# Optimization experiments

Measured on AMD Instinct MI355X. Metric: run time of the kernel, lower is better.

## Reference

```python
import jax, jax.numpy as jnp
import numpy as np

B, T, C = 2, 2048, 1024
N_HEAD = 16
HEAD_DIM = C // N_HEAD


def setup_inputs() -> dict:
    key = jax.random.key(0)
    k1, k2, k3, k4, k5 = jax.random.split(key, 5)
    s = 1.0 / np.sqrt(C)
    return {
        "x": jax.random.normal(k1, (B, T, C), dtype=jnp.float32),
        "w_attn": jax.random.normal(k2, (C, 3 * C), dtype=jnp.float32) * s,
        "b_attn": jax.random.normal(k3, (3 * C,), dtype=jnp.float32) * 0.02,
        "w_proj": jax.random.normal(k4, (C, C), dtype=jnp.float32) * s,
        "b_proj": jax.random.normal(k5, (C,), dtype=jnp.float32) * 0.02,
    }


def reference(x, w_attn, b_attn, w_proj, b_proj):
    Bx, Tx, Cx = x.shape
    qkv = x @ w_attn + b_attn  # [B, T, 3C]
    q, k, v = jnp.split(qkv, 3, axis=2)
    # [B, H, T, D]
    q = q.reshape(Bx, Tx, N_HEAD, HEAD_DIM).transpose(0, 2, 1, 3)
    k = k.reshape(Bx, Tx, N_HEAD, HEAD_DIM).transpose(0, 2, 1, 3)
    v = v.reshape(Bx, Tx, N_HEAD, HEAD_DIM).transpose(0, 2, 1, 3)
    scale = 1.0 / jnp.sqrt(jnp.asarray(HEAD_DIM, dtype=x.dtype))
    att = jnp.einsum("bhqd,bhkd->bhqk", q, k) * scale  # [B,H,T,T]
    causal = jnp.tril(jnp.ones((Tx, Tx), dtype=bool))
    att = jnp.where(causal[None, None, :, :], att, -jnp.inf)
    att = jax.nn.softmax(att, axis=-1)
    y = jnp.einsum("bhqk,bhkd->bhqd", att, v)  # [B,H,T,D]
    y = y.transpose(0, 2, 1, 3).reshape(Bx, Tx, Cx)
    return y @ w_proj + b_proj
```

## Files before the change

kernel.cpp:

```cpp
#include <hip/hip_runtime.h>
#include <hip/hip_bf16.h>
#include <stdint.h>

#define TT 2048
#define CC 1024
#define NH 16
#define HD 64
#define BT 4096

typedef float f32x4 __attribute__((ext_vector_type(4)));
typedef __bf16 bf16x8 __attribute__((ext_vector_type(8)));
typedef __bf16 bf16x4 __attribute__((ext_vector_type(4)));
typedef short sh4 __attribute__((ext_vector_type(4)));

#define MFMA(a, b, c) __builtin_amdgcn_mfma_f32_16x16x32_bf16((a), (b), (c), 0, 0, 0)
#define MFMA16(a, b, c) __builtin_amdgcn_mfma_f32_16x16x16bf16_1k((a), (b), (c), 0, 0, 0)

__device__ __forceinline__ void gload16(const void* g, void* l) {
    __builtin_amdgcn_global_load_lds(
        (const __attribute__((address_space(1))) void*)g,
        (__attribute__((address_space(3))) void*)l,
        16, 0, 0);
}

__global__ __launch_bounds__(256) void prep(
    const float* __restrict__ x, __bf16* __restrict__ xb,
    const float* __restrict__ wa, __bf16* __restrict__ oa,
    const float* __restrict__ wp, __bf16* __restrict__ op) {
    __shared__ float tile[32][33];
    int b0 = blockIdx.x;
    if (b0 < 1024) {
        int i = b0 * 256 + threadIdx.x;
        const int stride = 1024 * 256;
        const int n4 = BT * CC / 4;
        for (; i < n4; i += stride) {
            float4 v = reinterpret_cast<const float4*>(x)[i];
            bf16x4 o;
            o.x = (__bf16)v.x; o.y = (__bf16)v.y;
            o.z = (__bf16)v.z; o.w = (__bf16)v.w;
            reinterpret_cast<bf16x4*>(xb)[i] = o;
        }
    } else {
        int idx = b0 - 1024;
        int bx = idx & 127, r0 = (idx >> 7) * 32;
        const float* in;
        __bf16* out;
        int C;
        if (bx < 96) { in = wa; out = oa; C = 3072; }
        else         { in = wp; out = op; C = 1024; bx -= 96; }
        int c0 = bx * 32;
        int tx = threadIdx.x & 31, ty = (threadIdx.x >> 5) & 7;
#pragma unroll
        for (int j = 0; j < 32; j += 8)
            tile[ty + j][tx] = in[(size_t)(r0 + ty + j) * C + c0 + tx];
        __syncthreads();
#pragma unroll
        for (int j = 0; j < 32; j += 8)
            out[(size_t)(c0 + ty + j) * 1024 + r0 + tx] = (__bf16)tile[tx][ty + j];
    }
}

template <int MODE>
__global__ __launch_bounds__(256) void gemm128(
    const __bf16* __restrict__ A, const __bf16* __restrict__ Bt,
    const float* __restrict__ bias,
    __bf16* __restrict__ oq, __bf16* __restrict__ ok, __bf16* __restrict__ ov,
    float* __restrict__ of, int M, int N, int K) {
    __shared__ __align__(16) __bf16 As[128 * 64];
    __shared__ __align__(16) __bf16 Bs[128 * 64];
    const int tid = threadIdx.x;
    const int w = tid >> 6, lane = tid & 63;
    const int l15 = lane & 15, lg = lane >> 4;
    const int m0 = blockIdx.y * 128, n0 = blockIdx.x * 128;
    const int wr = w >> 1, wc = w & 1;

    const f32x4 zero4 = {0.f, 0.f, 0.f, 0.f};
    f32x4 acc[4][4];
#pragma unroll
    for (int m = 0; m < 4; ++m)
#pragma unroll
        for (int n = 0; n < 4; ++n) acc[m][n] = zero4;

    const char* Ab = (const char*)A;
    const char* Bb = (const char*)Bt;
    const size_t rowbytes = (size_t)K * 2;

    for (int kt = 0; kt < K; kt += 64) {
#pragma unroll
        for (int j = 0; j < 4; ++j) {
            int base = (w * 4 + j) * 1024;
            int d0 = base + lane * 16;
            int row = d0 >> 7;
            int colb = d0 & 127;
            int scolb = colb ^ ((row & 7) << 4);
            gload16(Ab + (size_t)(m0 + row) * rowbytes + (size_t)kt * 2 + scolb,
                    (char*)As + base);
            gload16(Bb + (size_t)(n0 + row) * rowbytes + (size_t)kt * 2 + scolb,
                    (char*)Bs + base);
        }
        __syncthreads();
#pragma unroll
        for (int kk = 0; kk < 2; ++kk) {
            bf16x8 af[4], bfr[4];
#pragma unroll
            for (int m = 0; m < 4; ++m) {
                int row = wr * 64 + m * 16 + l15;
                int colb = kk * 64 + lg * 16;
                af[m] = *(const bf16x8*)((const char*)As + row * 128 +
                                         (colb ^ ((row & 7) << 4)));
            }
#pragma unroll
            for (int n = 0; n < 4; ++n) {
                int row = wc * 64 + n * 16 + l15;
                int colb = kk * 64 + lg * 16;
                bfr[n] = *(const bf16x8*)((const char*)Bs + row * 128 +
                                          (colb ^ ((row & 7) << 4)));
            }
#pragma unroll
            for (int m = 0; m < 4; ++m)
#pragma unroll
                for (int n = 0; n < 4; ++n)
                    acc[m][n] = MFMA(af[m], bfr[n], acc[m][n]);
        }
        __syncthreads();
    }

#pragma unroll
    for (int n = 0; n < 4; ++n) {
        int col = n0 + wc * 64 + n * 16 + l15;
        float bs = bias[col];
        if constexpr (MODE == 0) {
            int sec = col >> 10;
            int cc = col & 1023;
            int h = cc >> 6, d = cc & 63;
            if (sec == 2) {
#pragma unroll
                for (int m = 0; m < 4; ++m) {
                    int rowb = m0 + wr * 64 + m * 16 + lg * 4;
                    int bb = rowb >> 11, t = rowb & 2047;
                    bf16x4 pk;
#pragma unroll
                    for (int r = 0; r < 4; ++r) pk[r] = (__bf16)(acc[m][n][r] + bs);
                    size_t base = ((size_t)(bb * NH + h) * HD + d) * (TT * 2);
                    size_t byte = base + (size_t)((t & ~63) * 2 +
                                   (((t & 63) * 2) ^ ((d & 15) << 3)));
                    *(bf16x4*)((char*)ov + byte) = pk;
                }
            } else {
                __bf16* dst = (sec == 0) ? oq : ok;
                float mult = (sec == 0) ? 0.125f * 1.44269504088896340736f : 1.0f;
#pragma unroll
                for (int m = 0; m < 4; ++m) {
                    int rowb = m0 + wr * 64 + m * 16 + lg * 4;
#pragma unroll
                    for (int r = 0; r < 4; ++r) {
                        int row = rowb + r;
                        int bb = row >> 11, t = row & 2047;
                        float val = (acc[m][n][r] + bs) * mult;
                        dst[((size_t)(bb * NH + h) * TT + t) * HD + d] = (__bf16)val;
                    }
                }
            }
        } else {
#pragma unroll
            for (int m = 0; m < 4; ++m) {
                int rowb = m0 + wr * 64 + m * 16 + lg * 4;
#pragma unroll
                for (int r = 0; r < 4; ++r) {
                    int row = rowb + r;
                    of[(size_t)row * N + col] = acc[m][n][r] + bs;
                }
            }
        }
    }
}

__global__ __launch_bounds__(256) void attn_kernel(
    const __bf16* __restrict__ q, const __bf16* __restrict__ k,
    const __bf16* __restrict__ vt, __bf16* __restrict__ y) {
    __shared__ __align__(16) __bf16 Kb[2][64 * 64];
    __shared__ __align__(16) __bf16 Vb[2][64 * 64];

    const int n = blockIdx.x;
    const int batch = n >> 8, a = (n >> 5) & 7;
    const int qt = (batch == 0) ? 31 - a : (batch == 1) ? 16 + a
                 : (batch == 2) ? 15 - a : a;
    const int bh = ((n & 7) << 2) | ((n >> 3) & 3);
    const int tid = threadIdx.x, w = tid >> 6, lane = tid & 63;
    const int l15 = lane & 15, lg = lane >> 4;
    const char* kh = (const char*)(k + (size_t)bh * TT * HD);
    const char* vh = (const char*)(vt + (size_t)bh * HD * TT);
    const __bf16* qh = q + (size_t)bh * TT * HD;
    const int qbw = qt * 64 + w * 16;

    const f32x4 zero4 = {0.f, 0.f, 0.f, 0.f};
    float lrun = 0.f;
    f32x4 oacc[4];
    bf16x8 qf[2];
#pragma unroll
    for (int f = 0; f < 4; ++f) oacc[f] = zero4;
#pragma unroll
    for (int kk = 0; kk < 2; ++kk)
        qf[kk] = *(const bf16x8*)&qh[(size_t)(qbw + l15) * HD + kk * 32 + lg * 8];

    auto stage = [&](int kvb, int buf) {
#pragma unroll
        for (int j = 0; j < 2; ++j) {
            int d0 = ((w * 2 + j) * 64 + lane) * 16;
            int row = d0 >> 7, colb = d0 & 127;
            gload16(kh + (size_t)(kvb + row) * 128 + (colb ^ ((row & 7) << 4)),
                    (char*)Kb[buf] + d0);
            gload16(vh + (size_t)row * (TT * 2) + (size_t)kvb * 2 + colb,
                    (char*)Vb[buf] + d0);
        }
    };

    stage(0, 0);
    __syncthreads();

    for (int g = 0; g <= qt; ++g) {
        const int cur = g & 1;
        if (g < qt) stage((g + 1) * 64, cur ^ 1);
        const int kb = g * 64;

        f32x4 s[4];
#pragma unroll
        for (int kf = 0; kf < 4; ++kf) s[kf] = zero4;
        __builtin_amdgcn_s_setprio(1);
#pragma unroll
        for (int kf = 0; kf < 4; ++kf) {
            int krow = kf * 16 + l15;
            const char* kr = (const char*)Kb[cur] + krow * 128;
            bf16x8 k0 = *(const bf16x8*)(kr + ((lg * 16) ^ ((krow & 7) << 4)));
            bf16x8 k1 = *(const bf16x8*)(kr + ((64 + lg * 16) ^ ((krow & 7) << 4)));
            s[kf] = MFMA(k0, qf[0], s[kf]);
            s[kf] = MFMA(k1, qf[1], s[kf]);
        }
        __builtin_amdgcn_s_setprio(0);
        if (g == qt) {
            const int qq = qbw + l15;
#pragma unroll
            for (int kf = 0; kf < 4; ++kf)
#pragma unroll
                for (int r = 0; r < 4; ++r) {
                    int kk_ = kb + kf * 16 + lg * 4 + r;
                    if (kk_ > qq) s[kf][r] = -1e30f;
                }
        }
        float ss = 0.f;
        sh4 pb[4];
#pragma unroll
        for (int kf = 0; kf < 4; ++kf) {
            bf16x4 pk;
#pragma unroll
            for (int r = 0; r < 4; ++r) {
                float p = exp2f(s[kf][r]);
                pk[r] = (__bf16)p;
                ss += p;
            }
            pb[kf] = __builtin_bit_cast(sh4, pk);
        }
        lrun += ss;
        __builtin_amdgcn_s_setprio(1);
#pragma unroll
        for (int kf = 0; kf < 4; ++kf) {
            int cb = (kf * 32 + lg * 8) ^ (l15 << 3);
#pragma unroll
            for (int f = 0; f < 4; ++f) {
                int vrow = f * 16 + l15;
                bf16x4 va = *(const bf16x4*)((const char*)Vb[cur] + vrow * 128 + cb);
                oacc[f] = MFMA16(__builtin_bit_cast(sh4, va), pb[kf], oacc[f]);
            }
        }
        __builtin_amdgcn_s_setprio(0);
        __syncthreads();
    }

    lrun += __shfl_xor(lrun, 16);
    lrun += __shfl_xor(lrun, 32);
    const int b = bh >> 4, h = bh & 15;
    float inv = 1.0f / lrun;
#pragma unroll
    for (int f = 0; f < 4; ++f) {
        bf16x4 pk;
#pragma unroll
        for (int r = 0; r < 4; ++r) pk[r] = (__bf16)(oacc[f][r] * inv);
        *(bf16x4*)&y[(size_t)(b * TT + qbw + l15) * CC + h * 64 + f * 16 +
                     lg * 4] = pk;
    }
}

extern "C" void kernel_launch(void* const* d_in, const int* in_sizes, int n_in,
                              void* d_out, int out_size, void* d_ws, size_t ws_size,
                              hipStream_t stream) {
    const float* x      = (const float*)d_in[0];
    const float* w_attn = (const float*)d_in[1];
    const float* b_attn = (const float*)d_in[2];
    const float* w_proj = (const float*)d_in[3];
    const float* b_proj = (const float*)d_in[4];
    float* out = (float*)d_out;

    char* ws = (char*)d_ws;
    size_t off = 0;
    auto alloc = [&](size_t bytes) {
        char* p = ws + off;
        off += (bytes + 255) & ~(size_t)255;
        return p;
    };
    __bf16* xb   = (__bf16*)alloc((size_t)BT * CC * 2);
    __bf16* watb = (__bf16*)alloc((size_t)3 * CC * CC * 2);
    __bf16* wptb = (__bf16*)alloc((size_t)CC * CC * 2);
    __bf16* qb   = (__bf16*)alloc((size_t)BT * CC * 2);
    __bf16* kbuf = (__bf16*)alloc((size_t)BT * CC * 2);
    __bf16* vtb  = (__bf16*)alloc((size_t)BT * CC * 2);
    __bf16* yb   = (__bf16*)alloc((size_t)BT * CC * 2);

    prep<<<5120, 256, 0, stream>>>(x, xb, w_attn, watb, w_proj, wptb);

    gemm128<0><<<dim3(3 * CC / 128, BT / 128), 256, 0, stream>>>(
        xb, watb, b_attn, qb, kbuf, vtb, nullptr, BT, 3 * CC, CC);

    attn_kernel<<<1024, 256, 0, stream>>>(qb, kbuf, vtb, yb);

    gemm128<1><<<dim3(CC / 128, BT / 128), 256, 0, stream>>>(
        yb, wptb, b_proj, nullptr, nullptr, nullptr, out, BT, CC, CC);
}
```

Before: 108.7 us.

## Process two query tiles per attention block to reuse staged K/V tiles

Each attention workgroup now handles a 128-row query tile split into two 64-row sub-tiles. Every K/V tile staged in shared memory is reused for both sub-tiles, which roughly halves K/V global loads and LDS reads per query row, and the grid drops from 1024 to 512 blocks. The cost is doubled accumulator and score register use, which may lower occupancy, and the diagonal tile now runs extra masked compute for the lower sub-tile. The block-to-tile ordering is changed to keep causal workloads balanced.

```diff
diff --git a/kernel.cpp b/kernel.cpp
--- a/kernel.cpp
+++ b/kernel.cpp
@@ -182,31 +182,35 @@
     __shared__ __align__(16) __bf16 Vb[2][64 * 64];
 
     const int n = blockIdx.x;
-    const int batch = n >> 8, a = (n >> 5) & 7;
-    const int qt = (batch == 0) ? 31 - a : (batch == 1) ? 16 + a
-                 : (batch == 2) ? 15 - a : a;
+    const int j = n >> 5;
+    const int qt2 = (j < 8) ? 15 - j : j - 8;
     const int bh = ((n & 7) << 2) | ((n >> 3) & 3);
     const int tid = threadIdx.x, w = tid >> 6, lane = tid & 63;
     const int l15 = lane & 15, lg = lane >> 4;
     const char* kh = (const char*)(k + (size_t)bh * TT * HD);
     const char* vh = (const char*)(vt + (size_t)bh * HD * TT);
     const __bf16* qh = q + (size_t)bh * TT * HD;
-    const int qbw = qt * 64 + w * 16;
+    const int qbw[2] = { qt2 * 128 + w * 16, qt2 * 128 + 64 + w * 16 };
+    const int nt = 2 * qt2 + 2;
 
     const f32x4 zero4 = {0.f, 0.f, 0.f, 0.f};
-    float lrun = 0.f;
-    f32x4 oacc[4];
-    bf16x8 qf[2];
-#pragma unroll
-    for (int f = 0; f < 4; ++f) oacc[f] = zero4;
-#pragma unroll
-    for (int kk = 0; kk < 2; ++kk)
-        qf[kk] = *(const bf16x8*)&qh[(size_t)(qbw + l15) * HD + kk * 32 + lg * 8];
+    float lrun[2] = {0.f, 0.f};
+    f32x4 oacc[2][4];
+    bf16x8 qf[2][2];
+#pragma unroll
+    for (int a = 0; a < 2; ++a) {
+#pragma unroll
+        for (int f = 0; f < 4; ++f) oacc[a][f] = zero4;
+#pragma unroll
+        for (int kk = 0; kk < 2; ++kk)
+            qf[a][kk] = *(const bf16x8*)&qh[(size_t)(qbw[a] + l15) * HD +
+                                           kk * 32 + lg * 8];
+    }
 
     auto stage = [&](int kvb, int buf) {
 #pragma unroll
-        for (int j = 0; j < 2; ++j) {
-            int d0 = ((w * 2 + j) * 64 + lane) * 16;
+        for (int jj = 0; jj < 2; ++jj) {
+            int d0 = ((w * 2 + jj) * 64 + lane) * 16;
             int row = d0 >> 7, colb = d0 & 127;
             gload16(kh + (size_t)(kvb + row) * 128 + (colb ^ ((row & 7) << 4)),
                     (char*)Kb[buf] + d0);
@@ -218,14 +222,16 @@
     stage(0, 0);
     __syncthreads();
 
-    for (int g = 0; g <= qt; ++g) {
+    for (int g = 0; g < nt; ++g) {
         const int cur = g & 1;
-        if (g < qt) stage((g + 1) * 64, cur ^ 1);
+        if (g + 1 < nt) stage((g + 1) * 64, cur ^ 1);
         const int kb = g * 64;
 
-        f32x4 s[4];
-#pragma unroll
-        for (int kf = 0; kf < 4; ++kf) s[kf] = zero4;
+        f32x4 s[2][4];
+#pragma unroll
+        for (int a = 0; a < 2; ++a)
+#pragma unroll
+            for (int kf = 0; kf < 4; ++kf) s[a][kf] = zero4;
         __builtin_amdgcn_s_setprio(1);
 #pragma unroll
         for (int kf = 0; kf < 4; ++kf) {
@@ -233,34 +239,42 @@
             const char* kr = (const char*)Kb[cur] + krow * 128;
             bf16x8 k0 = *(const bf16x8*)(kr + ((lg * 16) ^ ((krow & 7) << 4)));
             bf16x8 k1 = *(const bf16x8*)(kr + ((64 + lg * 16) ^ ((krow & 7) << 4)));
-            s[kf] = MFMA(k0, qf[0], s[kf]);
-            s[kf] = MFMA(k1, qf[1], s[kf]);
+            s[0][kf] = MFMA(k0, qf[0][0], s[0][kf]);
+            s[0][kf] = MFMA(k1, qf[0][1], s[0][kf]);
+            s[1][kf] = MFMA(k0, qf[1][0], s[1][kf]);
+            s[1][kf] = MFMA(k1, qf[1][1], s[1][kf]);
         }
         __builtin_amdgcn_s_setprio(0);
-        if (g == qt) {
-            const int qq = qbw + l15;
-#pragma unroll
-            for (int kf = 0; kf < 4; ++kf)
+#pragma unroll
+        for (int a = 0; a < 2; ++a) {
+            if (kb + 63 > qbw[a]) {
+                const int qq = qbw[a] + l15;
+#pragma unroll
+                for (int kf = 0; kf < 4; ++kf)
+#pragma unroll
+                    for (int r = 0; r < 4; ++r) {
+                        int kk_ = kb + kf * 16 + lg * 4 + r;
+                        if (kk_ > qq) s[a][kf][r] = -1e30f;
+                    }
+            }
+        }
+        sh4 pb[2][4];
+#pragma unroll
+        for (int a = 0; a < 2; ++a) {
+            float ss0 = 0.f, ss1 = 0.f;
+#pragma unroll
+            for (int kf = 0; kf < 4; ++kf) {
+                bf16x4 pk;
 #pragma unroll
                 for (int r = 0; r < 4; ++r) {
-                    int kk_ = kb + kf * 16 + lg * 4 + r;
-                    if (kk_ > qq) s[kf][r] = -1e30f;
+                    float p = exp2f(s[a][kf][r]);
+                    pk[r] = (__bf16)p;
+                    if (kf & 1) ss1 += p; else ss0 += p;
                 }
-        }
-        float ss = 0.f;
-        sh4 pb[4];
-#pragma unroll
-        for (int kf = 0; kf < 4; ++kf) {
-            bf16x4 pk;
-#pragma unroll
-            for (int r = 0; r < 4; ++r) {
-                float p = exp2f(s[kf][r]);
-                pk[r] = (__bf16)p;
-                ss += p;
-            }
-            pb[kf] = __builtin_bit_cast(sh4, pk);
-        }
-        lrun += ss;
+                pb[a][kf] = __builtin_bit_cast(sh4, pk);
+            }
+            lrun[a] += ss0 + ss1;
+        }
         __builtin_amdgcn_s_setprio(1);
 #pragma unroll
         for (int kf = 0; kf < 4; ++kf) {
@@ -269,24 +283,30 @@
             for (int f = 0; f < 4; ++f) {
                 int vrow = f * 16 + l15;
                 bf16x4 va = *(const bf16x4*)((const char*)Vb[cur] + vrow * 128 + cb);
-                oacc[f] = MFMA16(__builtin_bit_cast(sh4, va), pb[kf], oacc[f]);
+                sh4 vs = __builtin_bit_cast(sh4, va);
+                oacc[0][f] = MFMA16(vs, pb[0][kf], oacc[0][f]);
+                oacc[1][f] = MFMA16(vs, pb[1][kf], oacc[1][f]);
             }
         }
         __builtin_amdgcn_s_setprio(0);
         __syncthreads();
     }
 
-    lrun += __shfl_xor(lrun, 16);
-    lrun += __shfl_xor(lrun, 32);
     const int b = bh >> 4, h = bh & 15;
-    float inv = 1.0f / lrun;
-#pragma unroll
-    for (int f = 0; f < 4; ++f) {
-        bf16x4 pk;
-#pragma unroll
-        for (int r = 0; r < 4; ++r) pk[r] = (__bf16)(oacc[f][r] * inv);
-        *(bf16x4*)&y[(size_t)(b * TT + qbw + l15) * CC + h * 64 + f * 16 +
-                     lg * 4] = pk;
+#pragma unroll
+    for (int a = 0; a < 2; ++a) {
+        float lr = lrun[a];
+        lr += __shfl_xor(lr, 16);
+        lr += __shfl_xor(lr, 32);
+        float inv = 1.0f / lr;
+#pragma unroll
+        for (int f = 0; f < 4; ++f) {
+            bf16x4 pk;
+#pragma unroll
+            for (int r = 0; r < 4; ++r) pk[r] = (__bf16)(oacc[a][f][r] * inv);
+            *(bf16x4*)&y[(size_t)(b * TT + qbw[a] + l15) * CC + h * 64 + f * 16 +
+                         lg * 4] = pk;
+        }
     }
 }
 
@@ -320,7 +340,7 @@
     gemm128<0><<<dim3(3 * CC / 128, BT / 128), 256, 0, stream>>>(
         xb, watb, b_attn, qb, kbuf, vtb, nullptr, BT, 3 * CC, CC);
 
-    attn_kernel<<<1024, 256, 0, stream>>>(qb, kbuf, vtb, yb);
+    attn_kernel<<<512, 256, 0, stream>>>(qb, kbuf, vtb, yb);
 
     gemm128<1><<<dim3(CC / 128, BT / 128), 256, 0, stream>>>(
         yb, wptb, b_proj, nullptr, nullptr, nullptr, out, BT, CC, CC);
```

Result: slower. 128.8 us (+18.5%).

## Split heavy causal query tiles across two blocks and combine partial outputs

Applied to the files above, without the earlier changes.

Query tiles 16-31 have the longest causal KV ranges, and each is now split into two blocks that each cover half of the KV range. Each half writes unnormalized partial outputs and row sums to scratch space that reuses the xb/watb buffers. A new combine kernel sums the two halves and normalizes them. The aim is to balance load across the 1536 blocks and shorten the tail. In exchange it adds an extra launch, scratch traffic, and bf16 rounding of the partial sums. The split relies on the running softmax using no running max, so partial sums can simply be added.

```diff
diff --git a/kernel.cpp b/kernel.cpp
--- a/kernel.cpp
+++ b/kernel.cpp
@@ -177,15 +177,28 @@
 
 __global__ __launch_bounds__(256) void attn_kernel(
     const __bf16* __restrict__ q, const __bf16* __restrict__ k,
-    const __bf16* __restrict__ vt, __bf16* __restrict__ y) {
+    const __bf16* __restrict__ vt, __bf16* __restrict__ y,
+    __bf16* __restrict__ opart, float* __restrict__ lpart) {
     __shared__ __align__(16) __bf16 Kb[2][64 * 64];
     __shared__ __align__(16) __bf16 Vb[2][64 * 64];
 
     const int n = blockIdx.x;
-    const int batch = n >> 8, a = (n >> 5) & 7;
-    const int qt = (batch == 0) ? 31 - a : (batch == 1) ? 16 + a
-                 : (batch == 2) ? 15 - a : a;
     const int bh = ((n & 7) << 2) | ((n >> 3) & 3);
+    const int u = n >> 5;
+    int qt, g0, g1, half;
+    const bool heavy = (u < 32);
+    if (heavy) {
+        qt = 16 + (u >> 1);
+        half = u & 1;
+        int n0 = (qt + 2) >> 1;
+        g0 = half ? n0 : 0;
+        g1 = half ? qt + 1 : n0;
+    } else {
+        qt = 47 - u;
+        half = 0;
+        g0 = 0;
+        g1 = qt + 1;
+    }
     const int tid = threadIdx.x, w = tid >> 6, lane = tid & 63;
     const int l15 = lane & 15, lg = lane >> 4;
     const char* kh = (const char*)(k + (size_t)bh * TT * HD);
@@ -215,12 +228,12 @@
         }
     };
 
-    stage(0, 0);
+    stage(g0 * 64, 0);
     __syncthreads();
 
-    for (int g = 0; g <= qt; ++g) {
-        const int cur = g & 1;
-        if (g < qt) stage((g + 1) * 64, cur ^ 1);
+    for (int g = g0; g < g1; ++g) {
+        const int cur = (g - g0) & 1;
+        if (g + 1 < g1) stage((g + 1) * 64, cur ^ 1);
         const int kb = g * 64;
 
         f32x4 s[4];
@@ -278,16 +291,62 @@
 
     lrun += __shfl_xor(lrun, 16);
     lrun += __shfl_xor(lrun, 32);
-    const int b = bh >> 4, h = bh & 15;
-    float inv = 1.0f / lrun;
-#pragma unroll
-    for (int f = 0; f < 4; ++f) {
-        bf16x4 pk;
-#pragma unroll
-        for (int r = 0; r < 4; ++r) pk[r] = (__bf16)(oacc[f][r] * inv);
-        *(bf16x4*)&y[(size_t)(b * TT + qbw + l15) * CC + h * 64 + f * 16 +
-                     lg * 4] = pk;
-    }
+    if (heavy) {
+        size_t base = ((size_t)(bh * 16 + (qt - 16)) * 2 + half);
+        __bf16* op = opart + base * 4096;
+        float* lp = lpart + base * 64;
+        if (lg == 0) lp[w * 16 + l15] = lrun;
+#pragma unroll
+        for (int f = 0; f < 4; ++f) {
+            bf16x4 pk;
+#pragma unroll
+            for (int r = 0; r < 4; ++r) pk[r] = (__bf16)oacc[f][r];
+            *(bf16x4*)&op[(size_t)(w * 16 + l15) * 64 + f * 16 + lg * 4] = pk;
+        }
+    } else {
+        const int b = bh >> 4, h = bh & 15;
+        float inv = 1.0f / lrun;
+#pragma unroll
+        for (int f = 0; f < 4; ++f) {
+            bf16x4 pk;
+#pragma unroll
+            for (int r = 0; r < 4; ++r) pk[r] = (__bf16)(oacc[f][r] * inv);
+            *(bf16x4*)&y[(size_t)(b * TT + qbw + l15) * CC + h * 64 + f * 16 +
+                         lg * 4] = pk;
+        }
+    }
+}
+
+__global__ __launch_bounds__(256) void combine(
+    const __bf16* __restrict__ opart, const float* __restrict__ lpart,
+    __bf16* __restrict__ y) {
+    int n = blockIdx.x;
+    int bh = n & 31, qi = n >> 5;
+    int b = bh >> 4, h = bh & 15;
+    int qt = 16 + qi;
+    size_t base = ((size_t)(bh * 16 + qi)) * 2;
+    const __bf16* o0 = opart + base * 4096;
+    const __bf16* o1 = opart + (base + 1) * 4096;
+    const float* l0 = lpart + base * 64;
+    const float* l1 = l0 + 64;
+    int t = threadIdx.x;
+    int qq = t >> 2, dbase = (t & 3) * 16;
+    float inv = 1.0f / (l0[qq] + l1[qq]);
+    const __bf16* p0 = &o0[qq * 64 + dbase];
+    const __bf16* p1 = &o1[qq * 64 + dbase];
+    bf16x8 a0 = *(const bf16x8*)p0;
+    bf16x8 a1 = *(const bf16x8*)(p0 + 8);
+    bf16x8 c0 = *(const bf16x8*)p1;
+    bf16x8 c1 = *(const bf16x8*)(p1 + 8);
+    bf16x8 r0, r1;
+#pragma unroll
+    for (int i = 0; i < 8; ++i) {
+        r0[i] = (__bf16)(((float)a0[i] + (float)c0[i]) * inv);
+        r1[i] = (__bf16)(((float)a1[i] + (float)c1[i]) * inv);
+    }
+    __bf16* yp = &y[((size_t)(b * TT + qt * 64 + qq)) * CC + h * 64 + dbase];
+    *(bf16x8*)yp = r0;
+    *(bf16x8*)(yp + 8) = r1;
 }
 
 extern "C" void kernel_launch(void* const* d_in, const int* in_sizes, int n_in,
@@ -314,13 +373,17 @@
     __bf16* kbuf = (__bf16*)alloc((size_t)BT * CC * 2);
     __bf16* vtb  = (__bf16*)alloc((size_t)BT * CC * 2);
     __bf16* yb   = (__bf16*)alloc((size_t)BT * CC * 2);
+    __bf16* opart = xb;
+    float*  lpart = (float*)watb;
 
     prep<<<5120, 256, 0, stream>>>(x, xb, w_attn, watb, w_proj, wptb);
 
     gemm128<0><<<dim3(3 * CC / 128, BT / 128), 256, 0, stream>>>(
         xb, watb, b_attn, qb, kbuf, vtb, nullptr, BT, 3 * CC, CC);
 
-    attn_kernel<<<1024, 256, 0, stream>>>(qb, kbuf, vtb, yb);
+    attn_kernel<<<1536, 256, 0, stream>>>(qb, kbuf, vtb, yb, opart, lpart);
+
+    combine<<<512, 256, 0, stream>>>(opart, lpart, yb);
 
     gemm128<1><<<dim3(CC / 128, BT / 128), 256, 0, stream>>>(
         yb, wptb, b_proj, nullptr, nullptr, nullptr, out, BT, CC, CC);
```

Measured after the change: 109.8 us. About the same (+1.0%).
